# Kernel tuning notes

Measured on AMD Instinct MI355X. Metric: run time of the kernel, lower is better.

Reference implementation:

```python
import jax, jax.numpy as jnp
import numpy as np

N_BLOCKS = 5
D_HIDDEN = 512
D_LATENT = 512
NUM_FREQ = 10
IMG_H = IMG_W = 128


@jax.custom_vjp
def trunc_exp(x):
    return jnp.exp(x)

def _te_fwd(x):
    return jnp.exp(x), x

def _te_bwd(x, g):
    return (g * jnp.exp(jnp.clip(x, -15.0, 15.0)),)

trunc_exp.defvjp(_te_fwd, _te_bwd)


def setup_inputs() -> dict:
    key = jax.random.key(0)
    ks = jax.random.split(key, 12)
    cam, ray, samp = 2, 1024, 48
    world_xyz = jax.random.normal(ks[0], (cam, ray, samp, 3), jnp.float32) * 0.5
    world_xyz = world_xyz.at[..., 2].add(2.5)  # keep points in front of identity camera
    c2w = jnp.tile(jnp.eye(4, dtype=jnp.float32), (cam, 1, 1))
    k_mat = jnp.tile(jnp.array([[128.0, 0.0, 64.0], [0.0, 128.0, 64.0], [0.0, 0.0, 1.0]], jnp.float32), (cam, 1, 1))
    features = jax.random.normal(ks[1], (cam, D_LATENT, IMG_H, IMG_W), jnp.float32)
    s = 0.02
    d_in = 3 + 3 * 2 * NUM_FREQ  # 63
    return {
        'world_xyz': world_xyz,
        'c2w': c2w,
        'k_mat': k_mat,
        'features': features,
        'lin_in_w': jax.random.normal(ks[2], (d_in, D_HIDDEN), jnp.float32) * s,
        'lin_in_b': jnp.zeros((D_HIDDEN,), jnp.float32),
        'lin_z_w': jax.random.normal(ks[3], (N_BLOCKS, D_LATENT, D_HIDDEN), jnp.float32) * s,
        'lin_z_b': jnp.zeros((N_BLOCKS, D_HIDDEN), jnp.float32),
        'fc0_w': jax.random.normal(ks[4], (N_BLOCKS, D_HIDDEN, D_HIDDEN), jnp.float32) * s,
        'fc0_b': jnp.zeros((N_BLOCKS, D_HIDDEN), jnp.float32),
        'fc1_w': jax.random.normal(ks[5], (N_BLOCKS, D_HIDDEN, D_HIDDEN), jnp.float32) * s,
        'fc1_b': jnp.zeros((N_BLOCKS, D_HIDDEN), jnp.float32),
        'lin_out_w': jax.random.normal(ks[6], (D_HIDDEN, 1), jnp.float32) * s,
        'lin_out_b': jnp.zeros((1,), jnp.float32),
    }


def _bilinear(feat, uv):
    # feat: [C, H, W]; uv: [N, 2] pixel coords. Bilinear, border padding, align_corners=True.
    Hd, Wd = feat.shape[1], feat.shape[2]
    x = jnp.clip(uv[:, 0], 0.0, Wd - 1.0)
    y = jnp.clip(uv[:, 1], 0.0, Hd - 1.0)
    x0 = jnp.floor(x); y0 = jnp.floor(y)
    x0i = x0.astype(jnp.int32); y0i = y0.astype(jnp.int32)
    x1i = jnp.minimum(x0i + 1, Wd - 1); y1i = jnp.minimum(y0i + 1, Hd - 1)
    wx = x - x0; wy = y - y0
    f00 = feat[:, y0i, x0i]; f01 = feat[:, y0i, x1i]
    f10 = feat[:, y1i, x0i]; f11 = feat[:, y1i, x1i]
    out = (f00 * ((1 - wx) * (1 - wy)) + f01 * (wx * (1 - wy)) +
           f10 * ((1 - wx) * wy) + f11 * (wx * wy))
    return out.T  # [N, C]


def _forward(world_xyz, c2w, k_mat, features, lin_in_w, lin_in_b, lin_z_w, lin_z_b,
             fc0_w, fc0_b, fc1_w, fc1_b, lin_out_w, lin_out_b):
    B, R, S, _ = world_xyz.shape
    pts = world_xyz.reshape(B, R * S, 3)
    # world -> camera (w2c = inverse of rigid c2w)
    rot = c2w[:, :3, :3]
    trans = c2w[:, :3, 3]
    cam_xyz = jnp.einsum('bji,bnj->bni', rot, pts - trans[:, None])  # R^T (p - t)
    # project with intrinsics
    uvw = jnp.einsum('bij,bnj->bni', k_mat, cam_xyz)
    z = uvw[..., 2:3]
    z = jnp.where(jnp.abs(z) < 1e-6, 1e-6, z)
    uv = uvw[..., :2] / z  # [B, N, 2] pixel coords
    aligned = jax.vmap(_bilinear)(features, uv)  # [B, N, C]
    # NeRF positional encoding (include_input=True, freqs 2^0..2^9, scaled by 2*pi)
    freqs = 2.0 ** jnp.arange(NUM_FREQ, dtype=jnp.float32)
    scaled = (2.0 * jnp.pi) * cam_xyz[..., None] * freqs  # [B, N, 3, F]
    scaled = scaled.reshape(B, R * S, 3 * NUM_FREQ)
    enc = jnp.concatenate([cam_xyz, jnp.sin(scaled), jnp.cos(scaled)], axis=-1)  # [B, N, 63]
    # ResnetFC: lin_in then residual blocks with latent injection
    h = enc @ lin_in_w + lin_in_b
    for i in range(N_BLOCKS):
        h = h + aligned @ lin_z_w[i] + lin_z_b[i]
        net = jax.nn.relu(h) @ fc0_w[i] + fc0_b[i]
        dx = jax.nn.relu(net) @ fc1_w[i] + fc1_b[i]
        h = h + dx
    sigma = jax.nn.relu(h) @ lin_out_w + lin_out_b  # [B, N, 1]
    return trunc_exp(sigma).reshape(B, R, S, 1)


def reference(world_xyz, c2w, k_mat, features, lin_in_w, lin_in_b, lin_z_w, lin_z_b,
              fc0_w, fc0_b, fc1_w, fc1_b, lin_out_w, lin_out_b):
    return _forward(world_xyz, c2w, k_mat, features, lin_in_w, lin_in_b, lin_z_w, lin_z_b,
                    fc0_w, fc0_b, fc1_w, fc1_b, lin_out_w, lin_out_b)
```

## Files before the change

### kernel.cpp

```cpp
#include <hip/hip_runtime.h>

typedef __bf16 bf16_t;
typedef bf16_t bf16x8 __attribute__((ext_vector_type(8)));
typedef float f32x4 __attribute__((ext_vector_type(4)));
typedef unsigned short u16;

#define P_TOTAL 98304
#define PTS_PER_BATCH 49152

__device__ __forceinline__ u16 f2bs(float f){ bf16_t b=(bf16_t)f; return __builtin_bit_cast(u16,b); }

__device__ __forceinline__ void bar_lds(){
  asm volatile("s_waitcnt lgkmcnt(0)" ::: "memory");
  __builtin_amdgcn_s_barrier();
  __builtin_amdgcn_sched_barrier(0);
}

__global__ void k_wtrans15(const float* __restrict__ lz, const float* __restrict__ f0,
                           const float* __restrict__ f1, u16* __restrict__ dst){
  int kt = blockIdx.x, ns = blockIdx.y, z = blockIdx.z;
  const float* src = (z<5) ? (lz + (size_t)z*262144)
                   : (z<10 ? (f0 + (size_t)(z-5)*262144)
                           : (f1 + (size_t)(z-10)*262144));
  u16* d = dst + (size_t)z*262144 + (size_t)(ns*16 + kt)*1024;
  int l = threadIdx.x;
  int col = ns*32 + (l&15);
  int kr  = kt*32 + (l>>4)*8;
  #pragma unroll
  for (int nt=0;nt<2;nt++){
    bf16x8 o;
    #pragma unroll
    for (int j=0;j<8;j++) o[j] = (bf16_t)src[(size_t)(kr+j)*512 + col + nt*16];
    *(bf16x8*)(d + nt*512 + l*8) = o;
  }
}

__global__ void k_wtrans_in(const float* __restrict__ w, u16* __restrict__ dst){
  int kt = blockIdx.x, ns = blockIdx.y;
  u16* d = dst + (size_t)(ns*2 + kt)*1024;
  int l = threadIdx.x;
  int col = ns*32 + (l&15);
  int kr  = kt*32 + (l>>4)*8;
  #pragma unroll
  for (int nt=0;nt<2;nt++){
    bf16x8 o;
    #pragma unroll
    for (int j=0;j<8;j++){
      int k = kr + j;
      o[j] = (k < 63) ? (bf16_t)w[(size_t)k*512 + col + nt*16] : (bf16_t)0.f;
    }
    *(bf16x8*)(d + nt*512 + l*8) = o;
  }
}

__global__ void k_featT(const float* __restrict__ feat, u16* __restrict__ featT){
  int x = threadIdx.x;
  int c8 = blockIdx.x*8;
  int y = blockIdx.y, b = blockIdx.z;
  float v[8];
  #pragma unroll
  for (int j=0;j<8;j++)
    v[j] = feat[(((size_t)(b*512 + c8 + j))*128 + y)*128 + x];
  bf16x8 o;
  #pragma unroll
  for (int j=0;j<8;j++) o[j] = (bf16_t)v[j];
  *(bf16x8*)(featT + (((size_t)(b*128 + y))*128 + x)*512 + c8) = o;
}

__global__ __launch_bounds__(1024) void k_points(
    const float* __restrict__ world, const float* __restrict__ c2w,
    const float* __restrict__ kmat, const u16* __restrict__ featT,
    u16* __restrict__ alignedF, u16* __restrict__ encF){
  __shared__ u16 act[16*520];
  __shared__ u16 encs[16*72];
  int wid = threadIdx.x >> 6, lane = threadIdx.x & 63;
  int p0 = blockIdx.x*16;
  int gp = p0 + wid;
  int b = gp / PTS_PER_BATCH;
  const float* wp = world + (size_t)gp*3;
  float px = wp[0], py = wp[1], pz = wp[2];
  const float* cw = c2w + b*16;
  float dx = px - cw[3], dy = py - cw[7], dz = pz - cw[11];
  float cx = cw[0]*dx + cw[4]*dy + cw[8]*dz;
  float cy = cw[1]*dx + cw[5]*dy + cw[9]*dz;
  float cz = cw[2]*dx + cw[6]*dy + cw[10]*dz;
  const float* km = kmat + b*9;
  float u0 = km[0]*cx + km[1]*cy + km[2]*cz;
  float v0 = km[3]*cx + km[4]*cy + km[5]*cz;
  float zz = km[6]*cx + km[7]*cy + km[8]*cz;
  if (fabsf(zz) < 1e-6f) zz = 1e-6f;
  float uu = u0/zz, vv = v0/zz;
  float xf = fminf(fmaxf(uu, 0.f), 127.f);
  float yf = fminf(fmaxf(vv, 0.f), 127.f);
  float x0f = floorf(xf), y0f = floorf(yf);
  int x0 = (int)x0f, y0 = (int)y0f;
  int x1 = min(x0+1,127), y1 = min(y0+1,127);
  float wx = xf - x0f, wy = yf - y0f;
  float w00 = (1.f-wx)*(1.f-wy), w01 = wx*(1.f-wy), w10 = (1.f-wx)*wy, w11 = wx*wy;
  size_t fb = (size_t)b*128*128*512;
  int c8 = lane*8;
  const bf16x8 t00 = *(const bf16x8*)(featT + fb + (size_t)(y0*128+x0)*512 + c8);
  const bf16x8 t01 = *(const bf16x8*)(featT + fb + (size_t)(y0*128+x1)*512 + c8);
  const bf16x8 t10 = *(const bf16x8*)(featT + fb + (size_t)(y1*128+x0)*512 + c8);
  const bf16x8 t11 = *(const bf16x8*)(featT + fb + (size_t)(y1*128+x1)*512 + c8);
  bf16x8 o;
  #pragma unroll
  for (int j=0;j<8;j++){
    float r = (float)t00[j]*w00 + (float)t01[j]*w01 + (float)t10[j]*w10 + (float)t11[j]*w11;
    o[j] = (bf16_t)r;
  }
  *(bf16x8*)&act[wid*520 + lane*8] = o;
  float cam[3] = {cx, cy, cz};
  float e;
  if (lane < 3) e = cam[lane];
  else if (lane < 33){
    int i = (lane-3)/10, f = (lane-3)%10;
    e = sinf(6.2831855f * cam[i] * (float)(1<<f));
  } else if (lane < 63){
    int i = (lane-33)/10, f = (lane-33)%10;
    e = cosf(6.2831855f * cam[i] * (float)(1<<f));
  } else e = 0.f;
  encs[wid*72 + lane] = f2bs(e);
  __syncthreads();
  int t = threadIdx.x;
  int g = blockIdx.x & 3;
  size_t blk = (size_t)(blockIdx.x >> 2);
  {
    int kt = t>>6, lo = t&63, fm = lo&15, fk8 = lo>>4;
    bf16x8 v = *(const bf16x8*)&act[fm*520 + kt*32 + fk8*8];
    *(bf16x8*)(alignedF + blk*32768 + (size_t)(kt*4+g)*512 + lo*8) = v;
  }
  if (t < 128){
    int kt = t>>6, lo = t&63, fm = lo&15, fk8 = lo>>4;
    bf16x8 v = *(const bf16x8*)&encs[fm*72 + kt*32 + fk8*8];
    *(bf16x8*)(encF + blk*4096 + (size_t)(kt*4+g)*512 + lo*8) = v;
  }
}


#define MFMA_BF16 __builtin_amdgcn_mfma_f32_16x16x32_bf16

template<int NK>
__device__ __forceinline__ void gemm4(const u16* sB, const u16* __restrict__ apS,
                                      const u16* __restrict__ apN, int l, int START,
                                      f32x4 (&acc)[4][2], bf16x8 (&a)[2][2]){
  const u16* bp = sB + l*8;
  constexpr int M = NK - 1;
  int c0 = START & M;
  bf16x8 br0 = *(const bf16x8*)(bp + c0*2048);
  bf16x8 br1 = *(const bf16x8*)(bp + c0*2048 + 512);
  bf16x8 br2 = *(const bf16x8*)(bp + c0*2048 + 1024);
  bf16x8 br3 = *(const bf16x8*)(bp + c0*2048 + 1536);
  #pragma unroll 1
  for (int ib=0; ib<NK/2-1; ++ib){
    {
      const int i = 2*ib;
      __builtin_amdgcn_s_setprio(1);
      acc[0][0] = MFMA_BF16(a[0][0], br0, acc[0][0], 0,0,0);
      acc[0][1] = MFMA_BF16(a[0][1], br0, acc[0][1], 0,0,0);
      acc[1][0] = MFMA_BF16(a[0][0], br1, acc[1][0], 0,0,0);
      acc[1][1] = MFMA_BF16(a[0][1], br1, acc[1][1], 0,0,0);
      acc[2][0] = MFMA_BF16(a[0][0], br2, acc[2][0], 0,0,0);
      acc[2][1] = MFMA_BF16(a[0][1], br2, acc[2][1], 0,0,0);
      acc[3][0] = MFMA_BF16(a[0][0], br3, acc[3][0], 0,0,0);
      acc[3][1] = MFMA_BF16(a[0][1], br3, acc[3][1], 0,0,0);
      __builtin_amdgcn_s_setprio(0);
      int cn = (START + i + 1) & M;
      br0 = *(const bf16x8*)(bp + cn*2048);
      br1 = *(const bf16x8*)(bp + cn*2048 + 512);
      br2 = *(const bf16x8*)(bp + cn*2048 + 1024);
      br3 = *(const bf16x8*)(bp + cn*2048 + 1536);
      int ca = (START + i + 2) & M;
      a[0][0] = *(const bf16x8*)(apS + ca*1024);
      a[0][1] = *(const bf16x8*)(apS + ca*1024 + 512);
    }
    {
      const int i = 2*ib + 1;
      __builtin_amdgcn_s_setprio(1);
      acc[0][0] = MFMA_BF16(a[1][0], br0, acc[0][0], 0,0,0);
      acc[0][1] = MFMA_BF16(a[1][1], br0, acc[0][1], 0,0,0);
      acc[1][0] = MFMA_BF16(a[1][0], br1, acc[1][0], 0,0,0);
      acc[1][1] = MFMA_BF16(a[1][1], br1, acc[1][1], 0,0,0);
      acc[2][0] = MFMA_BF16(a[1][0], br2, acc[2][0], 0,0,0);
      acc[2][1] = MFMA_BF16(a[1][1], br2, acc[2][1], 0,0,0);
      acc[3][0] = MFMA_BF16(a[1][0], br3, acc[3][0], 0,0,0);
      acc[3][1] = MFMA_BF16(a[1][1], br3, acc[3][1], 0,0,0);
      __builtin_amdgcn_s_setprio(0);
      int cn = (START + i + 1) & M;
      br0 = *(const bf16x8*)(bp + cn*2048);
      br1 = *(const bf16x8*)(bp + cn*2048 + 512);
      br2 = *(const bf16x8*)(bp + cn*2048 + 1024);
      br3 = *(const bf16x8*)(bp + cn*2048 + 1536);
      int ca = (START + i + 2) & M;
      a[1][0] = *(const bf16x8*)(apS + ca*1024);
      a[1][1] = *(const bf16x8*)(apS + ca*1024 + 512);
    }
  }
  {
    __builtin_amdgcn_s_setprio(1);
    acc[0][0] = MFMA_BF16(a[0][0], br0, acc[0][0], 0,0,0);
    acc[0][1] = MFMA_BF16(a[0][1], br0, acc[0][1], 0,0,0);
    acc[1][0] = MFMA_BF16(a[0][0], br1, acc[1][0], 0,0,0);
    acc[1][1] = MFMA_BF16(a[0][1], br1, acc[1][1], 0,0,0);
    acc[2][0] = MFMA_BF16(a[0][0], br2, acc[2][0], 0,0,0);
    acc[2][1] = MFMA_BF16(a[0][1], br2, acc[2][1], 0,0,0);
    acc[3][0] = MFMA_BF16(a[0][0], br3, acc[3][0], 0,0,0);
    acc[3][1] = MFMA_BF16(a[0][1], br3, acc[3][1], 0,0,0);
    __builtin_amdgcn_s_setprio(0);
    int cn = (START + NK - 1) & M;
    br0 = *(const bf16x8*)(bp + cn*2048);
    br1 = *(const bf16x8*)(bp + cn*2048 + 512);
    br2 = *(const bf16x8*)(bp + cn*2048 + 1024);
    br3 = *(const bf16x8*)(bp + cn*2048 + 1536);
    int ca = START & 15;
    a[0][0] = *(const bf16x8*)(apN + ca*1024);
    a[0][1] = *(const bf16x8*)(apN + ca*1024 + 512);
  }
  {
    __builtin_amdgcn_s_setprio(1);
    acc[0][0] = MFMA_BF16(a[1][0], br0, acc[0][0], 0,0,0);
    acc[0][1] = MFMA_BF16(a[1][1], br0, acc[0][1], 0,0,0);
    acc[1][0] = MFMA_BF16(a[1][0], br1, acc[1][0], 0,0,0);
    acc[1][1] = MFMA_BF16(a[1][1], br1, acc[1][1], 0,0,0);
    acc[2][0] = MFMA_BF16(a[1][0], br2, acc[2][0], 0,0,0);
    acc[2][1] = MFMA_BF16(a[1][1], br2, acc[2][1], 0,0,0);
    acc[3][0] = MFMA_BF16(a[1][0], br3, acc[3][0], 0,0,0);
    acc[3][1] = MFMA_BF16(a[1][1], br3, acc[3][1], 0,0,0);
    __builtin_amdgcn_s_setprio(0);
    int ca = (START + 1) & 15;
    a[1][0] = *(const bf16x8*)(apN + ca*1024);
    a[1][1] = *(const bf16x8*)(apN + ca*1024 + 512);
  }
}

__device__ __forceinline__ void add_bias4(const float* __restrict__ bias, int wn32, int rq,
                                          f32x4 (&acc)[4][2]){
  #pragma unroll
  for (int nt=0; nt<2; ++nt){
    f32x4 bv = *(const f32x4*)&bias[wn32 + nt*16 + rq];
    #pragma unroll
    for (int bt=0; bt<4; ++bt)
      #pragma unroll
      for (int r=0; r<4; ++r)
        acc[bt][nt][r] += bv[r];
  }
}

__device__ __forceinline__ void write_relu4(u16* dst, int w, int fm, int fk8,
                                            f32x4 (&acc)[4][2]){
  u16* base = dst + w*2048 + (fk8>>1)*128 + fm*8 + (fk8&1)*4;
  #pragma unroll
  for (int bt=0; bt<4; ++bt)
    #pragma unroll
    for (int nt=0; nt<2; ++nt){
      u16 p0 = f2bs(fmaxf(acc[bt][nt][0], 0.f));
      u16 p1 = f2bs(fmaxf(acc[bt][nt][1], 0.f));
      u16 p2 = f2bs(fmaxf(acc[bt][nt][2], 0.f));
      u16 p3 = f2bs(fmaxf(acc[bt][nt][3], 0.f));
      uint2 v;
      v.x = (unsigned)p0 | ((unsigned)p1 << 16);
      v.y = (unsigned)p2 | ((unsigned)p3 << 16);
      *(uint2*)(base + bt*512 + nt*256) = v;
    }
}

__global__ __launch_bounds__(1024, 4) void k_net(
    const u16* __restrict__ alignedF, const u16* __restrict__ encF,
    const u16* __restrict__ wtin, const float* __restrict__ b_in,
    const u16* __restrict__ wts, const float* __restrict__ bz,
    const float* __restrict__ b0, const float* __restrict__ b1,
    const float* __restrict__ wout, const float* __restrict__ bout,
    float* __restrict__ out)
{
  __shared__ u16 bufA[32768];
  __shared__ u16 bufB[32768];
  const int t = threadIdx.x, w = t>>6, l = t&63;
  const int fm = l&15, fk8 = l>>4, rq = fk8*4;
  const int wn32 = w*32;
  const int START = (w>>3) << 3;

  uint4 sa[4];
  const uint4* srcA = (const uint4*)(alignedF + (size_t)blockIdx.x*32768);
  #pragma unroll
  for (int j=0;j<4;j++) sa[j] = srcA[j*1024 + t];
  uint4 sb = {0,0,0,0};
  const uint4* srcE = (const uint4*)(encF + (size_t)blockIdx.x*4096);
  if (t < 512) sb = srcE[t];

  const u16* apEl = wtin + (size_t)w*2048 + l*8;
  bf16x8 a[2][2];
  #pragma unroll
  for (int d=0; d<2; ++d){
    a[d][0] = *(const bf16x8*)(apEl + d*1024);
    a[d][1] = *(const bf16x8*)(apEl + d*1024 + 512);
  }

  #pragma unroll
  for (int j=0;j<4;j++) *((uint4*)bufA + j*1024 + t) = sa[j];
  if (t < 512) *((uint4*)bufB + t) = sb;
  bar_lds();

  f32x4 h[4][2] = {};
  gemm4<2>(bufB, apEl, wts + (size_t)w*16384 + l*8, l, START, h, a);
  add_bias4(b_in, wn32, rq, h);

  #pragma unroll 1
  for (int i=0;i<5;i++){
    const u16* apz  = wts + (size_t)i*262144      + (size_t)w*16384 + l*8;
    const u16* apf0 = wts + (size_t)(5+i)*262144  + (size_t)w*16384 + l*8;
    const u16* apf1 = wts + (size_t)(10+i)*262144 + (size_t)w*16384 + l*8;
    const u16* apzn = (i<4) ? (wts + (size_t)(i+1)*262144 + (size_t)w*16384 + l*8) : apEl;

    gemm4<16>(bufA, apz, apf0, l, START, h, a);
    add_bias4(bz + i*512, wn32, rq, h);
    bar_lds();
    write_relu4(bufB, w, fm, fk8, h);
    bar_lds();
    f32x4 acc[4][2] = {};
    gemm4<16>(bufB, apf0, apf1, l, START, acc, a);
    add_bias4(b0 + i*512, wn32, rq, acc);
    bar_lds();
    write_relu4(bufB, w, fm, fk8, acc);
    bar_lds();
    gemm4<16>(bufB, apf1, apzn, l, START, h, a);
    add_bias4(b1 + i*512, wn32, rq, h);
  }

  float s[4];
  {
    #pragma unroll
    for (int bt=0; bt<4; ++bt) s[bt] = 0.f;
    #pragma unroll
    for (int nt=0; nt<2; ++nt){
      f32x4 wv = *(const f32x4*)&wout[wn32 + nt*16 + rq];
      #pragma unroll
      for (int bt=0; bt<4; ++bt)
        #pragma unroll
        for (int r=0; r<4; ++r)
          s[bt] += fmaxf(h[bt][nt][r], 0.f) * wv[r];
    }
  }
  #pragma unroll
  for (int bt=0; bt<4; ++bt){
    s[bt] += __shfl_xor(s[bt], 16, 64);
    s[bt] += __shfl_xor(s[bt], 32, 64);
  }
  bar_lds();
  float* red = (float*)bufB;
  if (l < 16){
    #pragma unroll
    for (int bt=0; bt<4; ++bt)
      red[w*64 + bt*16 + l] = s[bt];
  }
  bar_lds();
  if (t < 64){
    float aa = bout[0];
    #pragma unroll
    for (int wv=0; wv<16; wv++) aa += red[wv*64 + t];
    out[blockIdx.x*64 + t] = expf(aa);
  }
}

extern "C" void kernel_launch(void* const* d_in, const int* in_sizes, int n_in,
                              void* d_out, int out_size, void* d_ws, size_t ws_size,
                              hipStream_t stream) {
  const float* world = (const float*)d_in[0];
  const float* c2w   = (const float*)d_in[1];
  const float* kmat  = (const float*)d_in[2];
  const float* feat  = (const float*)d_in[3];
  const float* w_in  = (const float*)d_in[4];
  const float* b_in  = (const float*)d_in[5];
  const float* w_z   = (const float*)d_in[6];
  const float* b_z   = (const float*)d_in[7];
  const float* w_f0  = (const float*)d_in[8];
  const float* b_f0  = (const float*)d_in[9];
  const float* w_f1  = (const float*)d_in[10];
  const float* b_f1  = (const float*)d_in[11];
  const float* w_out = (const float*)d_in[12];
  const float* b_out = (const float*)d_in[13];
  float* out = (float*)d_out;
  char* ws = (char*)d_ws;

  size_t off = 0;
  u16* wts   = (u16*)(ws + off); off += (size_t)15*262144*2;
  u16* wtin  = (u16*)(ws + off); off += (size_t)512*64*2;
  u16* featT = (u16*)(ws + off); off += (size_t)2*128*128*512*2;
  u16* alignedF = (u16*)(ws + off); off += (size_t)P_TOTAL*512*2;
  u16* encF  = (u16*)(ws + off); off += (size_t)P_TOTAL*64*2;

  k_wtrans15<<<dim3(16,16,15), 64, 0, stream>>>(w_z, w_f0, w_f1, wts);
  k_wtrans_in<<<dim3(2,16,1), 64, 0, stream>>>(w_in, wtin);
  k_featT<<<dim3(64,128,2), 128, 0, stream>>>(feat, featT);
  k_points<<<dim3(P_TOTAL/16), 1024, 0, stream>>>(world, c2w, kmat, featT, alignedF, encF);
  k_net<<<dim3(P_TOTAL/64), 1024, 0, stream>>>(alignedF, encF, wtin, b_in, wts,
      b_z, b_f0, b_f1, w_out, b_out, out);
}
```

Measured before the change: 857.9 us.

## Double-buffer LDS fragments in GEMM loop and load inputs via global_load_lds

The GEMM inner loop now double-buffers the B fragments from LDS, issuing the next k-step's loads before the current MFMA cluster so LDS latency hides behind compute. It also drops the per-wave staggered K start (START rotation), so all waves walk K in the same order. The initial activation and encoding tiles are copied straight from global memory into LDS with global_load_lds, with no register round trip. This adds register pressure for the extra fragment buffer, and removing the stagger may bring back LDS bank or L2 contention between waves.

```diff
diff --git a/kernel.cpp b/kernel.cpp
--- a/kernel.cpp
+++ b/kernel.cpp
@@ -14,6 +14,11 @@
   asm volatile("s_waitcnt lgkmcnt(0)" ::: "memory");
   __builtin_amdgcn_s_barrier();
   __builtin_amdgcn_sched_barrier(0);
+}
+
+__device__ __forceinline__ void gload_lds16(const u16* g, u16* l){
+  __builtin_amdgcn_global_load_lds((const __attribute__((address_space(1))) void*)g,
+                                   (__attribute__((address_space(3))) void*)l, 16, 0, 0);
 }
 
 __global__ void k_wtrans15(const float* __restrict__ lz, const float* __restrict__ f0,
@@ -138,98 +143,51 @@
 }
 
 
-#define MFMA_BF16 __builtin_amdgcn_mfma_f32_16x16x32_bf16
+#define MFMA_BF16(A,B,C) __builtin_amdgcn_mfma_f32_16x16x32_bf16(A,B,C,0,0,0)
+
+__device__ __forceinline__ void mfma_cluster(const bf16x8& a0, const bf16x8& a1,
+                                             const bf16x8* br, f32x4 (&acc)[4][2]){
+  __builtin_amdgcn_s_setprio(1);
+  #pragma unroll
+  for (int q=0;q<4;q++){
+    acc[q][0] = MFMA_BF16(a0, br[q], acc[q][0]);
+    acc[q][1] = MFMA_BF16(a1, br[q], acc[q][1]);
+  }
+  __builtin_amdgcn_s_setprio(0);
+}
 
 template<int NK>
-__device__ __forceinline__ void gemm4(const u16* sB, const u16* __restrict__ apS,
-                                      const u16* __restrict__ apN, int l, int START,
+__device__ __forceinline__ void gemm5(const u16* bp, const u16* __restrict__ apS,
+                                      const u16* __restrict__ apN,
                                       f32x4 (&acc)[4][2], bf16x8 (&a)[2][2]){
-  const u16* bp = sB + l*8;
-  constexpr int M = NK - 1;
-  int c0 = START & M;
-  bf16x8 br0 = *(const bf16x8*)(bp + c0*2048);
-  bf16x8 br1 = *(const bf16x8*)(bp + c0*2048 + 512);
-  bf16x8 br2 = *(const bf16x8*)(bp + c0*2048 + 1024);
-  bf16x8 br3 = *(const bf16x8*)(bp + c0*2048 + 1536);
+  bf16x8 br[2][4];
+  #pragma unroll
+  for (int q=0;q<4;q++) br[0][q] = *(const bf16x8*)(bp + q*512);
   #pragma unroll 1
-  for (int ib=0; ib<NK/2-1; ++ib){
-    {
-      const int i = 2*ib;
-      __builtin_amdgcn_s_setprio(1);
-      acc[0][0] = MFMA_BF16(a[0][0], br0, acc[0][0], 0,0,0);
-      acc[0][1] = MFMA_BF16(a[0][1], br0, acc[0][1], 0,0,0);
-      acc[1][0] = MFMA_BF16(a[0][0], br1, acc[1][0], 0,0,0);
-      acc[1][1] = MFMA_BF16(a[0][1], br1, acc[1][1], 0,0,0);
-      acc[2][0] = MFMA_BF16(a[0][0], br2, acc[2][0], 0,0,0);
-      acc[2][1] = MFMA_BF16(a[0][1], br2, acc[2][1], 0,0,0);
-      acc[3][0] = MFMA_BF16(a[0][0], br3, acc[3][0], 0,0,0);
-      acc[3][1] = MFMA_BF16(a[0][1], br3, acc[3][1], 0,0,0);
-      __builtin_amdgcn_s_setprio(0);
-      int cn = (START + i + 1) & M;
-      br0 = *(const bf16x8*)(bp + cn*2048);
-      br1 = *(const bf16x8*)(bp + cn*2048 + 512);
-      br2 = *(const bf16x8*)(bp + cn*2048 + 1024);
-      br3 = *(const bf16x8*)(bp + cn*2048 + 1536);
-      int ca = (START + i + 2) & M;
-      a[0][0] = *(const bf16x8*)(apS + ca*1024);
-      a[0][1] = *(const bf16x8*)(apS + ca*1024 + 512);
-    }
-    {
-      const int i = 2*ib + 1;
-      __builtin_amdgcn_s_setprio(1);
-      acc[0][0] = MFMA_BF16(a[1][0], br0, acc[0][0], 0,0,0);
-      acc[0][1] = MFMA_BF16(a[1][1], br0, acc[0][1], 0,0,0);
-      acc[1][0] = MFMA_BF16(a[1][0], br1, acc[1][0], 0,0,0);
-      acc[1][1] = MFMA_BF16(a[1][1], br1, acc[1][1], 0,0,0);
-      acc[2][0] = MFMA_BF16(a[1][0], br2, acc[2][0], 0,0,0);
-      acc[2][1] = MFMA_BF16(a[1][1], br2, acc[2][1], 0,0,0);
-      acc[3][0] = MFMA_BF16(a[1][0], br3, acc[3][0], 0,0,0);
-      acc[3][1] = MFMA_BF16(a[1][1], br3, acc[3][1], 0,0,0);
-      __builtin_amdgcn_s_setprio(0);
-      int cn = (START + i + 1) & M;
-      br0 = *(const bf16x8*)(bp + cn*2048);
-      br1 = *(const bf16x8*)(bp + cn*2048 + 512);
-      br2 = *(const bf16x8*)(bp + cn*2048 + 1024);
-      br3 = *(const bf16x8*)(bp + cn*2048 + 1536);
-      int ca = (START + i + 2) & M;
-      a[1][0] = *(const bf16x8*)(apS + ca*1024);
-      a[1][1] = *(const bf16x8*)(apS + ca*1024 + 512);
-    }
+  for (int kb=0; kb<NK/2-1; ++kb){
+    const u16* bk = bp  + kb*4096;
+    const u16* ak = apS + kb*2048;
+    #pragma unroll
+    for (int q=0;q<4;q++) br[1][q] = *(const bf16x8*)(bk + 2048 + q*512);
+    mfma_cluster(a[0][0], a[0][1], br[0], acc);
+    a[0][0] = *(const bf16x8*)(ak + 2048);
+    a[0][1] = *(const bf16x8*)(ak + 2048 + 512);
+    #pragma unroll
+    for (int q=0;q<4;q++) br[0][q] = *(const bf16x8*)(bk + 4096 + q*512);
+    mfma_cluster(a[1][0], a[1][1], br[1], acc);
+    a[1][0] = *(const bf16x8*)(ak + 3072);
+    a[1][1] = *(const bf16x8*)(ak + 3072 + 512);
   }
   {
-    __builtin_amdgcn_s_setprio(1);
-    acc[0][0] = MFMA_BF16(a[0][0], br0, acc[0][0], 0,0,0);
-    acc[0][1] = MFMA_BF16(a[0][1], br0, acc[0][1], 0,0,0);
-    acc[1][0] = MFMA_BF16(a[0][0], br1, acc[1][0], 0,0,0);
-    acc[1][1] = MFMA_BF16(a[0][1], br1, acc[1][1], 0,0,0);
-    acc[2][0] = MFMA_BF16(a[0][0], br2, acc[2][0], 0,0,0);
-    acc[2][1] = MFMA_BF16(a[0][1], br2, acc[2][1], 0,0,0);
-    acc[3][0] = MFMA_BF16(a[0][0], br3, acc[3][0], 0,0,0);
-    acc[3][1] = MFMA_BF16(a[0][1], br3, acc[3][1], 0,0,0);
-    __builtin_amdgcn_s_setprio(0);
-    int cn = (START + NK - 1) & M;
-    br0 = *(const bf16x8*)(bp + cn*2048);
-    br1 = *(const bf16x8*)(bp + cn*2048 + 512);
-    br2 = *(const bf16x8*)(bp + cn*2048 + 1024);
-    br3 = *(const bf16x8*)(bp + cn*2048 + 1536);
-    int ca = START & 15;
-    a[0][0] = *(const bf16x8*)(apN + ca*1024);
-    a[0][1] = *(const bf16x8*)(apN + ca*1024 + 512);
-  }
-  {
-    __builtin_amdgcn_s_setprio(1);
-    acc[0][0] = MFMA_BF16(a[1][0], br0, acc[0][0], 0,0,0);
-    acc[0][1] = MFMA_BF16(a[1][1], br0, acc[0][1], 0,0,0);
-    acc[1][0] = MFMA_BF16(a[1][0], br1, acc[1][0], 0,0,0);
-    acc[1][1] = MFMA_BF16(a[1][1], br1, acc[1][1], 0,0,0);
-    acc[2][0] = MFMA_BF16(a[1][0], br2, acc[2][0], 0,0,0);
-    acc[2][1] = MFMA_BF16(a[1][1], br2, acc[2][1], 0,0,0);
-    acc[3][0] = MFMA_BF16(a[1][0], br3, acc[3][0], 0,0,0);
-    acc[3][1] = MFMA_BF16(a[1][1], br3, acc[3][1], 0,0,0);
-    __builtin_amdgcn_s_setprio(0);
-    int ca = (START + 1) & 15;
-    a[1][0] = *(const bf16x8*)(apN + ca*1024);
-    a[1][1] = *(const bf16x8*)(apN + ca*1024 + 512);
+    const u16* bk = bp + (NK/2-1)*4096;
+    #pragma unroll
+    for (int q=0;q<4;q++) br[1][q] = *(const bf16x8*)(bk + 2048 + q*512);
+    mfma_cluster(a[0][0], a[0][1], br[0], acc);
+    a[0][0] = *(const bf16x8*)(apN);
+    a[0][1] = *(const bf16x8*)(apN + 512);
+    mfma_cluster(a[1][0], a[1][1], br[1], acc);
+    a[1][0] = *(const bf16x8*)(apN + 1024);
+    a[1][1] = *(const bf16x8*)(apN + 1536);
   }
 }
 
@@ -277,31 +235,28 @@
   const int t = threadIdx.x, w = t>>6, l = t&63;
   const int fm = l&15, fk8 = l>>4, rq = fk8*4;
   const int wn32 = w*32;
-  const int START = (w>>3) << 3;
-
-  uint4 sa[4];
-  const uint4* srcA = (const uint4*)(alignedF + (size_t)blockIdx.x*32768);
-  #pragma unroll
-  for (int j=0;j<4;j++) sa[j] = srcA[j*1024 + t];
-  uint4 sb = {0,0,0,0};
-  const uint4* srcE = (const uint4*)(encF + (size_t)blockIdx.x*4096);
-  if (t < 512) sb = srcE[t];
+
+  {
+    const u16* srcA = alignedF + (size_t)blockIdx.x*32768;
+    #pragma unroll
+    for (int j=0;j<4;j++)
+      gload_lds16(srcA + j*8192 + t*8, bufA + j*8192 + t*8);
+    if (t < 512){
+      const u16* srcE = encF + (size_t)blockIdx.x*4096;
+      gload_lds16(srcE + t*8, bufB + t*8);
+    }
+  }
+  asm volatile("s_waitcnt vmcnt(0)" ::: "memory");
+  __builtin_amdgcn_s_barrier();
+  __builtin_amdgcn_sched_barrier(0);
 
   const u16* apEl = wtin + (size_t)w*2048 + l*8;
   bf16x8 a[2][2];
-  #pragma unroll
-  for (int d=0; d<2; ++d){
-    a[d][0] = *(const bf16x8*)(apEl + d*1024);
-    a[d][1] = *(const bf16x8*)(apEl + d*1024 + 512);
-  }
-
-  #pragma unroll
-  for (int j=0;j<4;j++) *((uint4*)bufA + j*1024 + t) = sa[j];
-  if (t < 512) *((uint4*)bufB + t) = sb;
-  bar_lds();
+  a[0][0] = *(const bf16x8*)(apEl);        a[0][1] = *(const bf16x8*)(apEl + 512);
+  a[1][0] = *(const bf16x8*)(apEl + 1024); a[1][1] = *(const bf16x8*)(apEl + 1536);
 
   f32x4 h[4][2] = {};
-  gemm4<2>(bufB, apEl, wts + (size_t)w*16384 + l*8, l, START, h, a);
+  gemm5<2>(bufB + l*8, apEl, wts + (size_t)w*16384 + l*8, h, a);
   add_bias4(b_in, wn32, rq, h);
 
   #pragma unroll 1
@@ -311,18 +266,18 @@
     const u16* apf1 = wts + (size_t)(10+i)*262144 + (size_t)w*16384 + l*8;
     const u16* apzn = (i<4) ? (wts + (size_t)(i+1)*262144 + (size_t)w*16384 + l*8) : apEl;
 
-    gemm4<16>(bufA, apz, apf0, l, START, h, a);
+    gemm5<16>(bufA + l*8, apz, apf0, h, a);
     add_bias4(bz + i*512, wn32, rq, h);
     bar_lds();
     write_relu4(bufB, w, fm, fk8, h);
     bar_lds();
     f32x4 acc[4][2] = {};
-    gemm4<16>(bufB, apf0, apf1, l, START, acc, a);
+    gemm5<16>(bufB + l*8, apf0, apf1, acc, a);
     add_bias4(b0 + i*512, wn32, rq, acc);
     bar_lds();
     write_relu4(bufB, w, fm, fk8, acc);
     bar_lds();
-    gemm4<16>(bufB, apf1, apzn, l, START, h, a);
+    gemm5<16>(bufB + l*8, apf1, apzn, h, a);
     add_bias4(b1 + i*512, wn32, rq, h);
   }
 
```

Result: slower. 891.8 us (+4.0%).
